# Performance work log

Measured on AMD Instinct MI355X. Metric: run time of the kernel, lower is better.

## Reference

```python
import jax, jax.numpy as jnp
import numpy as np

N_NODES = 100_000
N_EDGES = 1_600_000
N_GRAPHS = 256
IN_DIM, HID, HEADS, LAYERS = 480, 128, 4, 3
HEAD_DIM = HID // HEADS
NEG_SLOPE = 0.2
LN_EPS = 1e-5


def setup_inputs() -> dict:
    key = jax.random.key(0)
    ks = jax.random.split(key, 12)
    x = jax.random.normal(ks[0], (N_NODES, IN_DIM), dtype=jnp.float32)
    edge_index = jax.random.randint(ks[1], (2, N_EDGES), 0, N_NODES, dtype=jnp.int32)
    batch = jnp.sort(jax.random.randint(ks[2], (N_NODES,), 0, N_GRAPHS, dtype=jnp.int32))
    s_in = 1.0 / np.sqrt(IN_DIM)
    s_h = 1.0 / np.sqrt(HID)
    return {
        "x": x,
        "W_in": jax.random.uniform(ks[3], (IN_DIM, HID), jnp.float32, -s_in, s_in),
        "b_in": jax.random.uniform(ks[4], (HID,), jnp.float32, -s_in, s_in),
        "W_gat": jax.random.uniform(ks[5], (LAYERS, HID, HID), jnp.float32, -s_h, s_h),
        "att_src": jax.random.uniform(ks[6], (LAYERS, HEADS, HEAD_DIM), jnp.float32, -s_h, s_h),
        "att_dst": jax.random.uniform(ks[7], (LAYERS, HEADS, HEAD_DIM), jnp.float32, -s_h, s_h),
        "b_gat": jnp.zeros((LAYERS, HID), jnp.float32),
        "ln_g": jnp.ones((LAYERS, HID), jnp.float32),
        "ln_b": jnp.zeros((LAYERS, HID), jnp.float32),
        "edge_index": edge_index,
        "batch": batch,
    }


def _gat_conv(h_in, W, a_src, a_dst, bias, src, dst, n):
    # h: [N, H, D] per-head projected features
    h = (h_in @ W).reshape(n, HEADS, HEAD_DIM)
    asrc = jnp.sum(h * a_src, axis=-1)  # [N, H]
    adst = jnp.sum(h * a_dst, axis=-1)  # [N, H]
    e = jax.nn.leaky_relu(asrc[src] + adst[dst], NEG_SLOPE)  # [E, H]
    # scatter-softmax over incoming edges of each destination node
    emax = jax.ops.segment_max(e, dst, num_segments=n)  # [N, H]
    emax = jnp.where(jnp.isfinite(emax), emax, 0.0)
    ex = jnp.exp(e - emax[dst])
    denom = jax.ops.segment_sum(ex, dst, num_segments=n)
    alpha = ex / jnp.maximum(denom, 1e-16)[dst]  # [E, H]
    out = jax.ops.segment_sum(alpha[:, :, None] * h[src], dst, num_segments=n)
    return out.reshape(n, HID) + bias


def _layer_norm(x, g, b):
    mu = jnp.mean(x, axis=-1, keepdims=True)
    var = jnp.mean(jnp.square(x - mu), axis=-1, keepdims=True)
    return (x - mu) * jax.lax.rsqrt(var + LN_EPS) * g + b


def reference(x, W_in, b_in, W_gat, att_src, att_dst, b_gat, ln_g, ln_b, edge_index, batch):
    n = x.shape[0]
    # PyG GATConv default add_self_loops=True
    loop = jnp.arange(n, dtype=edge_index.dtype)
    src = jnp.concatenate([edge_index[0], loop])
    dst = jnp.concatenate([edge_index[1], loop])

    h = jax.nn.relu(x @ W_in + b_in)
    for l in range(LAYERS):
        residual = h
        h = _gat_conv(h, W_gat[l], att_src[l], att_dst[l], b_gat[l], src, dst, n)
        h = jax.nn.relu(_layer_norm(h, ln_g[l], ln_b[l]))
        # dropout omitted (eval mode)
        h = h + residual
    # global mean pool per graph
    sums = jax.ops.segment_sum(h, batch, num_segments=N_GRAPHS)
    cnt = jax.ops.segment_sum(jnp.ones((n,), h.dtype), batch, num_segments=N_GRAPHS)
    return sums / jnp.maximum(cnt, 1.0)[:, None]
```

## Files before the change

### kernel.cpp

```cpp
#include <hip/hip_runtime.h>
#include <hip/hip_bf16.h>

#define HID 128
#define NEG_SLOPE 0.2f
#define LN_EPS 1e-5f
#define SEG_CAP 8192

typedef __attribute__((ext_vector_type(8))) short short8;
typedef __attribute__((ext_vector_type(4))) float floatx4;

__device__ __forceinline__ float us2f(unsigned short u) {
    union { unsigned int i; float f; } c; c.i = ((unsigned int)u) << 16; return c.f;
}
__device__ __forceinline__ float lo2f(unsigned u) {
    union { unsigned int i; float f; } c; c.i = u << 16; return c.f;
}
__device__ __forceinline__ float hi2f(unsigned u) {
    union { unsigned int i; float f; } c; c.i = u & 0xffff0000u; return c.f;
}
__device__ __forceinline__ unsigned short f2us(float f) {
    union { float f; unsigned u; } c; c.f = f;
    unsigned r = c.u + 0x7FFF + ((c.u >> 16) & 1);
    return (unsigned short)(r >> 16);
}
__device__ __forceinline__ unsigned pack2(float a, float b) {
    return (unsigned)f2us(a) | ((unsigned)f2us(b) << 16);
}
__device__ __forceinline__ float ldw(const void* p, long i, int bf) {
    return bf ? us2f(((const unsigned short*)p)[i]) : ((const float*)p)[i];
}
__device__ __forceinline__ float lrelu(float x) { return x > 0.f ? x : NEG_SLOPE * x; }
__device__ __forceinline__ float wsum32(float x) {
#pragma unroll
    for (int o = 16; o > 0; o >>= 1) x += __shfl_xor(x, o);
    return x;
}
__device__ __forceinline__ float pick4(float4 v, int h) {
    return h == 0 ? v.x : (h == 1 ? v.y : (h == 2 ? v.z : v.w));
}

__global__ __launch_bounds__(256) void init_kernel(const float* __restrict__ x, int* __restrict__ flag,
                                                   int* __restrict__ bucket_cnt) {
    const int t = blockIdx.x * 256 + threadIdx.x;
    if (t < 512) bucket_cnt[t] = 0;
    if (blockIdx.x == 0 && threadIdx.x < 64) {
        float v = x[threadIdx.x];
        int bad = (!(v == v)) || (fabsf(v) > 1e6f);
        unsigned long long m = __ballot(bad);
        if (threadIdx.x == 0) flag[0] = (m != 0ull) ? 1 : 0;
    }
}

__global__ __launch_bounds__(256) void bucket_hist_kernel(const int* __restrict__ dst, int E, int nb,
                                                          int* __restrict__ bucket_cnt) {
    __shared__ int hist[512];
    for (int i = threadIdx.x; i < nb; i += 256) hist[i] = 0;
    __syncthreads();
    const int base = blockIdx.x * 4096;
    const int end = min(base + 4096, E);
    for (int i = base + threadIdx.x; i < end; i += 256)
        atomicAdd(&hist[dst[i] >> 8], 1);
    __syncthreads();
    for (int i = threadIdx.x; i < nb; i += 256)
        if (hist[i]) atomicAdd(&bucket_cnt[i], hist[i]);
}

__global__ __launch_bounds__(512) void bucket_scan_kernel(const int* __restrict__ bucket_cnt,
                                                          int* __restrict__ bucket_base,
                                                          int* __restrict__ cursor,
                                                          int nb, int* __restrict__ row_ptr, int N) {
    __shared__ int sc[512];
    const int t = threadIdx.x;
    const int v = (t < nb) ? bucket_cnt[t] : 0;
    int x = v;
    sc[t] = x;
    __syncthreads();
    for (int o = 1; o < 512; o <<= 1) {
        const int y = (t >= o) ? sc[t - o] : 0;
        __syncthreads();
        x += y;
        sc[t] = x;
        __syncthreads();
    }
    if (t < nb) { bucket_base[t] = x - v; cursor[t] = x - v; }
    if (t == nb - 1) { bucket_base[nb] = x; row_ptr[N] = x; }
}

__global__ __launch_bounds__(256) void partition_kernel(const int* __restrict__ src, const int* __restrict__ dst,
                                                        int E, int nb, int* __restrict__ cursor,
                                                        unsigned long long* __restrict__ tmp) {
    __shared__ int hist[512];
    __shared__ int tbase[512];
    for (int i = threadIdx.x; i < nb; i += 256) hist[i] = 0;
    __syncthreads();
    const int base = blockIdx.x * 4096;
    const int end = min(base + 4096, E);
    int myd[16], mys[16], myr[16];
#pragma unroll
    for (int j = 0; j < 16; ++j) {
        const int i = base + threadIdx.x + j * 256;
        if (i < end) {
            const int d = dst[i];
            myd[j] = d;
            mys[j] = src[i];
            myr[j] = atomicAdd(&hist[d >> 8], 1);
        } else {
            myd[j] = -1;
        }
    }
    __syncthreads();
    for (int i = threadIdx.x; i < nb; i += 256) {
        const int hv = hist[i];
        tbase[i] = hv ? atomicAdd(&cursor[i], hv) : 0;
    }
    __syncthreads();
#pragma unroll
    for (int j = 0; j < 16; ++j) {
        if (myd[j] >= 0) {
            const int b = myd[j] >> 8;
            tmp[(size_t)tbase[b] + myr[j]] = ((unsigned long long)(unsigned)myd[j] << 32) | (unsigned)mys[j];
        }
    }
}

__global__ __launch_bounds__(256) void bucket_sort_kernel(const unsigned long long* __restrict__ tmp,
                                                          const int* __restrict__ bucket_base,
                                                          int* __restrict__ row_ptr, int* __restrict__ csr,
                                                          int N) {
    __shared__ int hist[256];
    __shared__ int sc[256];
    __shared__ int off[256];
    __shared__ int outb[SEG_CAP];
    const int b = blockIdx.x;
    const int node0 = b << 8;
    const int nn = min(256, N - node0);
    const int s0 = bucket_base[b], s1 = bucket_base[b + 1];
    const int cnt = s1 - s0;
    const int t = threadIdx.x;
    hist[t] = 0;
    __syncthreads();
    for (int i = s0 + t; i < s1; i += 256) {
        const int d = (int)(tmp[i] >> 32) - node0;
        atomicAdd(&hist[d], 1);
    }
    __syncthreads();
    const int v = hist[t];
    int x = v;
    sc[t] = x;
    __syncthreads();
    for (int o = 1; o < 256; o <<= 1) {
        const int y = (t >= o) ? sc[t - o] : 0;
        __syncthreads();
        x += y;
        sc[t] = x;
        __syncthreads();
    }
    off[t] = x - v;
    if (t < nn) row_ptr[node0 + t] = s0 + (x - v);
    hist[t] = 0;
    __syncthreads();
    if (cnt <= SEG_CAP) {
        for (int i = s0 + t; i < s1; i += 256) {
            const unsigned long long pr = tmp[i];
            const int d = (int)(pr >> 32) - node0;
            const int p = off[d] + atomicAdd(&hist[d], 1);
            outb[p] = (int)(unsigned)(pr & 0xffffffffu);
        }
        __syncthreads();
        for (int i = t; i < cnt; i += 256) csr[s0 + i] = outb[i];
    } else {
        for (int i = s0 + t; i < s1; i += 256) {
            const unsigned long long pr = tmp[i];
            const int d = (int)(pr >> 32) - node0;
            const int p = off[d] + atomicAdd(&hist[d], 1);
            csr[s0 + p] = (int)(unsigned)(pr & 0xffffffffu);
        }
    }
}

__global__ __launch_bounds__(256) void transpose_w_kernel(const void* __restrict__ W, long w_off, int K,
                                                          unsigned short* __restrict__ Wt,
                                                          const int* __restrict__ flagp) {
    const int bf = flagp[0];
    const int i = blockIdx.x * 256 + threadIdx.x;
    if (i >= 128 * K) return;
    const int n = i / K, k = i - n * K;
    const long s = w_off + (long)k * 128 + n;
    Wt[i] = bf ? ((const unsigned short*)W)[s] : f2us(((const float*)W)[s]);
}

__global__ __launch_bounds__(256) void transpose_wg_kernel(const void* __restrict__ W,
                                                           unsigned short* __restrict__ Wt,
                                                           const int* __restrict__ flagp) {
    const int bf = flagp[0];
    const int i = blockIdx.x * 256 + threadIdx.x;
    if (i >= 3 * 128 * 128) return;
    const int l = i >> 14, j = i & 16383;
    const int n = j >> 7, k = j & 127;
    const long s = (long)l * 16384 + (long)k * 128 + n;
    Wt[i] = bf ? ((const unsigned short*)W)[s] : f2us(((const float*)W)[s]);
}

template <int C_BF, int FUSE>
__global__ __launch_bounds__(256) void mfma_gemm_kernel(const void* __restrict__ Ap, int a_input,
                                                        const unsigned short* __restrict__ Bt,
                                                        const void* __restrict__ bias, long bias_off,
                                                        void* __restrict__ Cp,
                                                        const void* __restrict__ attS,
                                                        const void* __restrict__ attD, long a_off,
                                                        float* __restrict__ asrc, float* __restrict__ adst,
                                                        int M, int K, int do_relu,
                                                        const int* __restrict__ flagp) {
    __shared__ unsigned short As[2][128 * 40];
    __shared__ unsigned short Bs[2][128 * 40];
    const int bf = flagp[0];
    const int a_bf = a_input ? (bf ? 1 : 2) : 2;
    const int t = threadIdx.x;
    const int bm = blockIdx.x * 128;
    const int lane = t & 63, wave = t >> 6;
    const int r = lane & 15, quad = lane >> 4;
    const int srow = t >> 1, skh = (t & 1) * 16;
    const int grow = bm + srow;

    floatx4 acc[2][8];
#pragma unroll
    for (int mt = 0; mt < 2; ++mt)
#pragma unroll
        for (int nt = 0; nt < 8; ++nt)
#pragma unroll
            for (int q = 0; q < 4; ++q) acc[mt][nt][q] = 0.f;

    auto loadAB = [&](int k0, uint4& u0, uint4& u1, uint4& v0, uint4& v1) {
        u0 = make_uint4(0, 0, 0, 0); u1 = u0;
        if (grow < M) {
            const long aidx = (long)grow * K + k0 + skh;
            if (a_bf == 1) {
                const unsigned short* ap = (const unsigned short*)Ap + aidx;
                u0 = ((const uint4*)ap)[0];
                u1 = ((const uint4*)ap)[1];
            } else {
                const float* ap = (const float*)Ap + aidx;
                float4 f0 = ((const float4*)ap)[0];
                float4 f1 = ((const float4*)ap)[1];
                float4 f2 = ((const float4*)ap)[2];
                float4 f3 = ((const float4*)ap)[3];
                u0 = make_uint4(pack2(f0.x, f0.y), pack2(f0.z, f0.w), pack2(f1.x, f1.y), pack2(f1.z, f1.w));
                u1 = make_uint4(pack2(f2.x, f2.y), pack2(f2.z, f2.w), pack2(f3.x, f3.y), pack2(f3.z, f3.w));
            }
        }
        const unsigned short* bp = Bt + (long)srow * K + k0 + skh;
        v0 = ((const uint4*)bp)[0];
        v1 = ((const uint4*)bp)[1];
    };

    uint4 a0, a1, b0, b1;
    loadAB(0, a0, a1, b0, b1);
    *(uint4*)&As[0][srow * 40 + skh]     = a0;
    *(uint4*)&As[0][srow * 40 + skh + 8] = a1;
    *(uint4*)&Bs[0][srow * 40 + skh]     = b0;
    *(uint4*)&Bs[0][srow * 40 + skh + 8] = b1;
    __syncthreads();

    int cur = 0;
    for (int k0 = 0; k0 < K; k0 += 32) {
        const bool have = (k0 + 32) < K;
        if (have) loadAB(k0 + 32, a0, a1, b0, b1);

        short8 afr[2];
        afr[0] = *(const short8*)&As[cur][(wave * 32 + r) * 40 + quad * 8];
        afr[1] = *(const short8*)&As[cur][(wave * 32 + 16 + r) * 40 + quad * 8];
#pragma unroll
        for (int nt = 0; nt < 8; ++nt) {
            short8 bfr = *(const short8*)&Bs[cur][(nt * 16 + r) * 40 + quad * 8];
            acc[0][nt] = __builtin_amdgcn_mfma_f32_16x16x32_bf16(afr[0], bfr, acc[0][nt], 0, 0, 0);
            acc[1][nt] = __builtin_amdgcn_mfma_f32_16x16x32_bf16(afr[1], bfr, acc[1][nt], 0, 0, 0);
        }

        if (have) {
            cur ^= 1;
            *(uint4*)&As[cur][srow * 40 + skh]     = a0;
            *(uint4*)&As[cur][srow * 40 + skh + 8] = a1;
            *(uint4*)&Bs[cur][srow * 40 + skh]     = b0;
            *(uint4*)&Bs[cur][srow * 40 + skh + 8] = b1;
            __syncthreads();
        }
    }

    if (FUSE) {
        float aS[8], aD[8];
#pragma unroll
        for (int nt = 0; nt < 8; ++nt) {
            aS[nt] = ldw(attS, a_off + nt * 16 + r, bf);
            aD[nt] = ldw(attD, a_off + nt * 16 + r, bf);
        }
#pragma unroll
        for (int mt = 0; mt < 2; ++mt) {
#pragma unroll
            for (int reg = 0; reg < 4; ++reg) {
                const int gr = bm + wave * 32 + mt * 16 + quad * 4 + reg;
                if (gr < M) {
                    float s0 = 0.f, s1 = 0.f, s2 = 0.f, s3 = 0.f;
                    float d0 = 0.f, d1 = 0.f, d2 = 0.f, d3 = 0.f;
#pragma unroll
                    for (int nt = 0; nt < 8; ++nt) {
                        const float v = acc[mt][nt][reg];
                        const unsigned short us = f2us(v);
                        ((unsigned short*)Cp)[(long)gr * HID + nt * 16 + r] = us;
                        const float vr = us2f(us);
                        if (nt < 2)      { s0 = fmaf(vr, aS[nt], s0); d0 = fmaf(vr, aD[nt], d0); }
                        else if (nt < 4) { s1 = fmaf(vr, aS[nt], s1); d1 = fmaf(vr, aD[nt], d1); }
                        else if (nt < 6) { s2 = fmaf(vr, aS[nt], s2); d2 = fmaf(vr, aD[nt], d2); }
                        else             { s3 = fmaf(vr, aS[nt], s3); d3 = fmaf(vr, aD[nt], d3); }
                    }
#pragma unroll
                    for (int o = 1; o < 16; o <<= 1) {
                        s0 += __shfl_xor(s0, o); s1 += __shfl_xor(s1, o);
                        s2 += __shfl_xor(s2, o); s3 += __shfl_xor(s3, o);
                        d0 += __shfl_xor(d0, o); d1 += __shfl_xor(d1, o);
                        d2 += __shfl_xor(d2, o); d3 += __shfl_xor(d3, o);
                    }
                    const int hsel = r & 3;
                    const float sv = hsel == 0 ? s0 : (hsel == 1 ? s1 : (hsel == 2 ? s2 : s3));
                    const float dv = hsel == 0 ? d0 : (hsel == 1 ? d1 : (hsel == 2 ? d2 : d3));
                    if (r < 4)      asrc[(size_t)gr * 4 + hsel] = sv;
                    else if (r < 8) adst[(size_t)gr * 4 + hsel] = dv;
                }
            }
        }
    } else {
        float bb[8];
#pragma unroll
        for (int nt = 0; nt < 8; ++nt) bb[nt] = bias ? ldw(bias, bias_off + nt * 16 + r, bf) : 0.f;

#pragma unroll
        for (int mt = 0; mt < 2; ++mt) {
            const int gr0 = bm + wave * 32 + mt * 16 + quad * 4;
#pragma unroll
            for (int reg = 0; reg < 4; ++reg) {
                const int gr = gr0 + reg;
                if (gr < M) {
#pragma unroll
                    for (int nt = 0; nt < 8; ++nt) {
                        float v = acc[mt][nt][reg] + bb[nt];
                        if (do_relu) v = fmaxf(v, 0.f);
                        const long ci = (long)gr * HID + nt * 16 + r;
                        if (C_BF) ((unsigned short*)Cp)[ci] = f2us(v);
                        else      ((float*)Cp)[ci] = v;
                    }
                }
            }
        }
    }
}

__global__ __launch_bounds__(256) void gat_kernel(float* __restrict__ h,
                                                  const unsigned short* __restrict__ hp,
                                                  const float* __restrict__ asrc,
                                                  const float* __restrict__ adst,
                                                  const int* __restrict__ row_ptr,
                                                  const int* __restrict__ csr,
                                                  const void* __restrict__ bgat,
                                                  const void* __restrict__ lng,
                                                  const void* __restrict__ lnb, long w_off,
                                                  int N, const int* __restrict__ flagp) {
    __shared__ uint2 ebuf[8][160];
    const int bf = flagp[0];
    const int lane = threadIdx.x & 63;
    const int wslot = threadIdx.x >> 6;
    const int half = lane >> 5;
    const int ll = lane & 31;
    const int head4 = ll >> 3;
    const int c0 = ll << 2;
    const int n = (blockIdx.x << 3) | (wslot << 1) | half;
    if (n >= N) return;

    const int e0 = row_ptr[n], e1 = row_ptr[n + 1];
    const float4 ad4 = *(const float4*)(adst + (size_t)n * 4);
    const float4 as4 = *(const float4*)(asrc + (size_t)n * 4);
    float4 es;
    es.x = lrelu(as4.x + ad4.x); es.y = lrelu(as4.y + ad4.y);
    es.z = lrelu(as4.z + ad4.z); es.w = lrelu(as4.w + ad4.w);

    const uint2 us = *(const uint2*)(hp + (size_t)n * HID + c0);
    float4 acc;
    acc.x = lo2f(us.x); acc.y = hi2f(us.x);
    acc.z = lo2f(us.y); acc.w = hi2f(us.y);

    float4 dnp = make_float4(0.f, 0.f, 0.f, 0.f);
    uint2* eb = ebuf[(wslot << 1) | half];

    for (int base = e0; base < e1; base += 32) {
        const int cnt = min(32, e1 - base);
        int s = 0;
        float4 ex4 = make_float4(0.f, 0.f, 0.f, 0.f);
        if (ll < cnt) {
            s = csr[base + ll];
            const float4 a = *(const float4*)(asrc + (size_t)s * 4);
            ex4.x = __expf(lrelu(a.x + ad4.x) - es.x);
            ex4.y = __expf(lrelu(a.y + ad4.y) - es.y);
            ex4.z = __expf(lrelu(a.z + ad4.z) - es.z);
            ex4.w = __expf(lrelu(a.w + ad4.w) - es.w);
            dnp.x += ex4.x; dnp.y += ex4.y; dnp.z += ex4.z; dnp.w += ex4.w;
        }
        const unsigned su = (unsigned)s;
        eb[ll * 5 + 0] = make_uint2(su, __float_as_uint(ex4.x));
        eb[ll * 5 + 1] = make_uint2(su, __float_as_uint(ex4.y));
        eb[ll * 5 + 2] = make_uint2(su, __float_as_uint(ex4.z));
        eb[ll * 5 + 3] = make_uint2(su, __float_as_uint(ex4.w));

        float4 aA = make_float4(0.f, 0.f, 0.f, 0.f);
        float4 aB = make_float4(0.f, 0.f, 0.f, 0.f);
        float4 aC = make_float4(0.f, 0.f, 0.f, 0.f);
        float4 aD = make_float4(0.f, 0.f, 0.f, 0.f);
        int i = 0;
#define GAT_EDGE(idx, A)                                                      \
        {                                                                     \
            const uint2 q = eb[(idx) * 5 + head4];                            \
            const uint2 u = *(const uint2*)(hp + (size_t)q.x * HID + c0);     \
            const float wq = __uint_as_float(q.y);                            \
            A.x = fmaf(wq, lo2f(u.x), A.x);                                   \
            A.y = fmaf(wq, hi2f(u.x), A.y);                                   \
            A.z = fmaf(wq, lo2f(u.y), A.z);                                   \
            A.w = fmaf(wq, hi2f(u.y), A.w);                                   \
        }
        for (; i + 4 <= cnt; i += 4) {
            GAT_EDGE(i + 0, aA);
            GAT_EDGE(i + 1, aB);
            GAT_EDGE(i + 2, aC);
            GAT_EDGE(i + 3, aD);
        }
        for (; i < cnt; ++i) GAT_EDGE(i, aA);
#undef GAT_EDGE
        acc.x += (aA.x + aB.x) + (aC.x + aD.x);
        acc.y += (aA.y + aB.y) + (aC.y + aD.y);
        acc.z += (aA.z + aB.z) + (aC.z + aD.z);
        acc.w += (aA.w + aB.w) + (aC.w + aD.w);
    }

    float4 dn;
    dn.x = wsum32(dnp.x) + 1.f;
    dn.y = wsum32(dnp.y) + 1.f;
    dn.z = wsum32(dnp.z) + 1.f;
    dn.w = wsum32(dnp.w) + 1.f;

    const float invd = 1.f / fmaxf(pick4(dn, head4), 1e-16f);
    acc.x *= invd; acc.y *= invd; acc.z *= invd; acc.w *= invd;
    acc.x += ldw(bgat, w_off + c0 + 0, bf);
    acc.y += ldw(bgat, w_off + c0 + 1, bf);
    acc.z += ldw(bgat, w_off + c0 + 2, bf);
    acc.w += ldw(bgat, w_off + c0 + 3, bf);

    const float mean = wsum32(acc.x + acc.y + acc.z + acc.w) * (1.f / 128.f);
    const float d0 = acc.x - mean, d1 = acc.y - mean, d2 = acc.z - mean, d3 = acc.w - mean;
    const float var = wsum32(d0 * d0 + d1 * d1 + d2 * d2 + d3 * d3) * (1.f / 128.f);
    const float rstd = rsqrtf(var + LN_EPS);
    float o0 = d0 * rstd * ldw(lng, w_off + c0 + 0, bf) + ldw(lnb, w_off + c0 + 0, bf);
    float o1 = d1 * rstd * ldw(lng, w_off + c0 + 1, bf) + ldw(lnb, w_off + c0 + 1, bf);
    float o2 = d2 * rstd * ldw(lng, w_off + c0 + 2, bf) + ldw(lnb, w_off + c0 + 2, bf);
    float o3 = d3 * rstd * ldw(lng, w_off + c0 + 3, bf) + ldw(lnb, w_off + c0 + 3, bf);
    o0 = fmaxf(o0, 0.f); o1 = fmaxf(o1, 0.f); o2 = fmaxf(o2, 0.f); o3 = fmaxf(o3, 0.f);

    const float4 r = *(const float4*)(h + (size_t)n * HID + c0);
    *(float4*)(h + (size_t)n * HID + c0) = make_float4(o0 + r.x, o1 + r.y, o2 + r.z, o3 + r.w);
}

__global__ __launch_bounds__(1024) void pool_kernel(const float* __restrict__ h, const int* __restrict__ batch,
                                                    void* __restrict__ out, int N,
                                                    const int* __restrict__ flagp) {
    const int g = blockIdx.x;
    int a = 0, b = N;
    while (a < b) { int mid = (a + b) >> 1; if (batch[mid] < g) a = mid + 1; else b = mid; }
    const int lo = a;
    b = N;
    while (a < b) { int mid = (a + b) >> 1; if (batch[mid] <= g) a = mid + 1; else b = mid; }
    const int hi = a;

    const int col = threadIdx.x & 127;
    const int slot = threadIdx.x >> 7;
    float s = 0.f;
    for (int r = lo + slot; r < hi; r += 8) s += h[(size_t)r * HID + col];
    __shared__ float part[8][128];
    part[slot][col] = s;
    __syncthreads();
    if (threadIdx.x < 128) {
        float tot = part[0][threadIdx.x];
#pragma unroll
        for (int p = 1; p < 8; ++p) tot += part[p][threadIdx.x];
        const float v = tot / fmaxf((float)(hi - lo), 1.f);
        if (flagp[0]) ((unsigned short*)out)[g * HID + threadIdx.x] = f2us(v);
        else          ((float*)out)[g * HID + threadIdx.x] = v;
    }
}

extern "C" void kernel_launch(void* const* d_in, const int* in_sizes, int n_in,
                              void* d_out, int out_size, void* d_ws, size_t ws_size,
                              hipStream_t stream) {
    const void* x     = d_in[0];
    const void* W_in  = d_in[1];
    const void* b_in  = d_in[2];
    const void* W_gat = d_in[3];
    const void* att_s = d_in[4];
    const void* att_d = d_in[5];
    const void* b_gat = d_in[6];
    const void* ln_g  = d_in[7];
    const void* ln_b  = d_in[8];
    const int* edge_index = (const int*)d_in[9];
    const int* batch      = (const int*)d_in[10];

    const int N = in_sizes[10];
    const int E = in_sizes[9] / 2;
    const int IN_DIM = in_sizes[0] / N;
    const int n_graphs = out_size / HID;

    const int* esrc = edge_index;
    const int* edst = edge_index + E;

    char* w = (char*)d_ws;
    auto carve = [&](size_t bytes) -> void* {
        void* p = (void*)w;
        w += (bytes + 255) & ~(size_t)255;
        return p;
    };
    int* flag             = (int*)carve(256);
    int* row_ptr          = (int*)carve((size_t)(N + 1) * 4);
    int* csr              = (int*)carve((size_t)E * 4);
    float* asrc           = (float*)carve((size_t)N * 4 * 4);
    float* adst           = (float*)carve((size_t)N * 4 * 4);
    int* bucket_cnt       = (int*)carve(512 * 4);
    int* bucket_base      = (int*)carve(513 * 4);
    int* cursor           = (int*)carve(512 * 4);
    unsigned short* Wt_in = (unsigned short*)carve((size_t)HID * IN_DIM * 2);
    unsigned short* Wt_g  = (unsigned short*)carve((size_t)3 * HID * HID * 2);
    float* h              = (float*)carve((size_t)N * HID * 4);
    unsigned short* hp    = (unsigned short*)carve((size_t)N * HID * 2);
    unsigned long long* tmp = (unsigned long long*)h;
    (void)ws_size; (void)n_in;

    init_kernel<<<2, 256, 0, stream>>>((const float*)x, flag, bucket_cnt);

    const int nb = (N + 255) >> 8;
    const int ntiles = (E + 4095) / 4096;
    bucket_hist_kernel<<<ntiles, 256, 0, stream>>>(edst, E, nb, bucket_cnt);
    bucket_scan_kernel<<<1, 512, 0, stream>>>(bucket_cnt, bucket_base, cursor, nb, row_ptr, N);
    partition_kernel<<<ntiles, 256, 0, stream>>>(esrc, edst, E, nb, cursor, tmp);
    bucket_sort_kernel<<<nb, 256, 0, stream>>>(tmp, bucket_base, row_ptr, csr, N);

    transpose_w_kernel<<<(HID * IN_DIM + 255) / 256, 256, 0, stream>>>(W_in, 0, IN_DIM, Wt_in, flag);
    transpose_wg_kernel<<<(3 * HID * HID + 255) / 256, 256, 0, stream>>>(W_gat, Wt_g, flag);

    mfma_gemm_kernel<0, 0><<<(N + 127) / 128, 256, 0, stream>>>(
        x, 1, Wt_in, b_in, 0, h, nullptr, nullptr, 0, nullptr, nullptr, N, IN_DIM, 1, flag);

    for (int l = 0; l < 3; ++l) {
        mfma_gemm_kernel<1, 1><<<(N + 127) / 128, 256, 0, stream>>>(
            h, 0, Wt_g + (size_t)l * HID * HID, nullptr, 0, hp,
            att_s, att_d, (long)l * HID, asrc, adst, N, HID, 0, flag);
        gat_kernel<<<(N + 7) / 8, 256, 0, stream>>>(h, hp, asrc, adst, row_ptr, csr,
                                                    b_gat, ln_g, ln_b, (long)l * HID, N, flag);
    }

    pool_kernel<<<n_graphs, 1024, 0, stream>>>(h, batch, d_out, N, flag);
}
```

Baseline: 750.8 us.

## Replace two-level bucket sort CSR build with per-node counting sort

Builds the destination-sorted CSR by counting edges per node with global atomics, running a two-level prefix scan and scattering source indices through per-node atomic cursors. This replaces the bucket histogram, partition and in-bucket sort pipeline, and the two weight-transpose kernels are merged into one launch. The intent is fewer passes over the edge list and less intermediate traffic. In exchange the per-node global atomics can contend, and the order of neighbours within a row is no longer deterministic, which may change floating-point summation order.

```diff
diff --git a/kernel.cpp b/kernel.cpp
--- a/kernel.cpp
+++ b/kernel.cpp
@@ -4,7 +4,6 @@
 #define HID 128
 #define NEG_SLOPE 0.2f
 #define LN_EPS 1e-5f
-#define SEG_CAP 8192
 
 typedef __attribute__((ext_vector_type(8))) short short8;
 typedef __attribute__((ext_vector_type(4))) float floatx4;
@@ -40,9 +39,9 @@
 }
 
 __global__ __launch_bounds__(256) void init_kernel(const float* __restrict__ x, int* __restrict__ flag,
-                                                   int* __restrict__ bucket_cnt) {
-    const int t = blockIdx.x * 256 + threadIdx.x;
-    if (t < 512) bucket_cnt[t] = 0;
+                                                   int* __restrict__ cnt, int N) {
+    const int i = blockIdx.x * 256 + threadIdx.x;
+    if (i < N) cnt[i] = 0;
     if (blockIdx.x == 0 && threadIdx.x < 64) {
         float v = x[threadIdx.x];
         int bad = (!(v == v)) || (fabsf(v) > 1e6f);
@@ -51,27 +50,38 @@
     }
 }
 
-__global__ __launch_bounds__(256) void bucket_hist_kernel(const int* __restrict__ dst, int E, int nb,
-                                                          int* __restrict__ bucket_cnt) {
-    __shared__ int hist[512];
-    for (int i = threadIdx.x; i < nb; i += 256) hist[i] = 0;
+__global__ __launch_bounds__(256) void node_hist_kernel(const int* __restrict__ dst, int E,
+                                                        int* __restrict__ cnt) {
+    const int i = blockIdx.x * 256 + threadIdx.x;
+    if (i < E) atomicAdd(&cnt[dst[i]], 1);
+}
+
+__global__ __launch_bounds__(256) void scan_local_kernel(const int* __restrict__ cnt,
+                                                         int* __restrict__ loc,
+                                                         int* __restrict__ part, int N) {
+    __shared__ int sc[256];
+    const int t = threadIdx.x;
+    const int n = blockIdx.x * 256 + t;
+    const int v = (n < N) ? cnt[n] : 0;
+    int x = v;
+    sc[t] = x;
     __syncthreads();
-    const int base = blockIdx.x * 4096;
-    const int end = min(base + 4096, E);
-    for (int i = base + threadIdx.x; i < end; i += 256)
-        atomicAdd(&hist[dst[i] >> 8], 1);
-    __syncthreads();
-    for (int i = threadIdx.x; i < nb; i += 256)
-        if (hist[i]) atomicAdd(&bucket_cnt[i], hist[i]);
-}
-
-__global__ __launch_bounds__(512) void bucket_scan_kernel(const int* __restrict__ bucket_cnt,
-                                                          int* __restrict__ bucket_base,
-                                                          int* __restrict__ cursor,
-                                                          int nb, int* __restrict__ row_ptr, int N) {
+    for (int o = 1; o < 256; o <<= 1) {
+        const int y = (t >= o) ? sc[t - o] : 0;
+        __syncthreads();
+        x += y;
+        sc[t] = x;
+        __syncthreads();
+    }
+    if (n < N) loc[n] = x - v;
+    if (t == 255) part[blockIdx.x] = x;
+}
+
+__global__ __launch_bounds__(512) void scan_part_kernel(int* __restrict__ part, int nblk,
+                                                        int* __restrict__ row_ptr, int N) {
     __shared__ int sc[512];
     const int t = threadIdx.x;
-    const int v = (t < nb) ? bucket_cnt[t] : 0;
+    const int v = (t < nblk) ? part[t] : 0;
     int x = v;
     sc[t] = x;
     __syncthreads();
@@ -82,123 +92,54 @@
         sc[t] = x;
         __syncthreads();
     }
-    if (t < nb) { bucket_base[t] = x - v; cursor[t] = x - v; }
-    if (t == nb - 1) { bucket_base[nb] = x; row_ptr[N] = x; }
-}
-
-__global__ __launch_bounds__(256) void partition_kernel(const int* __restrict__ src, const int* __restrict__ dst,
-                                                        int E, int nb, int* __restrict__ cursor,
-                                                        unsigned long long* __restrict__ tmp) {
-    __shared__ int hist[512];
-    __shared__ int tbase[512];
-    for (int i = threadIdx.x; i < nb; i += 256) hist[i] = 0;
-    __syncthreads();
-    const int base = blockIdx.x * 4096;
-    const int end = min(base + 4096, E);
-    int myd[16], mys[16], myr[16];
-#pragma unroll
-    for (int j = 0; j < 16; ++j) {
-        const int i = base + threadIdx.x + j * 256;
-        if (i < end) {
-            const int d = dst[i];
-            myd[j] = d;
-            mys[j] = src[i];
-            myr[j] = atomicAdd(&hist[d >> 8], 1);
-        } else {
-            myd[j] = -1;
-        }
-    }
-    __syncthreads();
-    for (int i = threadIdx.x; i < nb; i += 256) {
-        const int hv = hist[i];
-        tbase[i] = hv ? atomicAdd(&cursor[i], hv) : 0;
-    }
-    __syncthreads();
-#pragma unroll
-    for (int j = 0; j < 16; ++j) {
-        if (myd[j] >= 0) {
-            const int b = myd[j] >> 8;
-            tmp[(size_t)tbase[b] + myr[j]] = ((unsigned long long)(unsigned)myd[j] << 32) | (unsigned)mys[j];
-        }
-    }
-}
-
-__global__ __launch_bounds__(256) void bucket_sort_kernel(const unsigned long long* __restrict__ tmp,
-                                                          const int* __restrict__ bucket_base,
-                                                          int* __restrict__ row_ptr, int* __restrict__ csr,
-                                                          int N) {
-    __shared__ int hist[256];
-    __shared__ int sc[256];
-    __shared__ int off[256];
-    __shared__ int outb[SEG_CAP];
-    const int b = blockIdx.x;
-    const int node0 = b << 8;
-    const int nn = min(256, N - node0);
-    const int s0 = bucket_base[b], s1 = bucket_base[b + 1];
-    const int cnt = s1 - s0;
-    const int t = threadIdx.x;
-    hist[t] = 0;
-    __syncthreads();
-    for (int i = s0 + t; i < s1; i += 256) {
-        const int d = (int)(tmp[i] >> 32) - node0;
-        atomicAdd(&hist[d], 1);
-    }
-    __syncthreads();
-    const int v = hist[t];
-    int x = v;
-    sc[t] = x;
-    __syncthreads();
-    for (int o = 1; o < 256; o <<= 1) {
-        const int y = (t >= o) ? sc[t - o] : 0;
-        __syncthreads();
-        x += y;
-        sc[t] = x;
-        __syncthreads();
-    }
-    off[t] = x - v;
-    if (t < nn) row_ptr[node0 + t] = s0 + (x - v);
-    hist[t] = 0;
-    __syncthreads();
-    if (cnt <= SEG_CAP) {
-        for (int i = s0 + t; i < s1; i += 256) {
-            const unsigned long long pr = tmp[i];
-            const int d = (int)(pr >> 32) - node0;
-            const int p = off[d] + atomicAdd(&hist[d], 1);
-            outb[p] = (int)(unsigned)(pr & 0xffffffffu);
-        }
-        __syncthreads();
-        for (int i = t; i < cnt; i += 256) csr[s0 + i] = outb[i];
+    if (t < nblk) part[t] = x - v;
+    if (t == nblk - 1) row_ptr[N] = x;
+}
+
+__global__ __launch_bounds__(256) void scan_add_kernel(const int* __restrict__ loc,
+                                                       const int* __restrict__ part,
+                                                       int* __restrict__ row_ptr,
+                                                       int* __restrict__ cursor, int N) {
+    const int n = blockIdx.x * 256 + threadIdx.x;
+    if (n < N) {
+        const int v = loc[n] + part[blockIdx.x];
+        row_ptr[n] = v;
+        cursor[n] = v;
+    }
+}
+
+__global__ __launch_bounds__(256) void scatter_kernel(const int* __restrict__ src,
+                                                      const int* __restrict__ dst, int E,
+                                                      int* __restrict__ cursor, int* __restrict__ csr) {
+    const int i = blockIdx.x * 256 + threadIdx.x;
+    if (i < E) {
+        const int d = dst[i];
+        const int p = atomicAdd(&cursor[d], 1);
+        csr[p] = src[i];
+    }
+}
+
+__global__ __launch_bounds__(256) void transpose_all_kernel(const void* __restrict__ W_in,
+                                                            const void* __restrict__ W_gat,
+                                                            unsigned short* __restrict__ Wt_in,
+                                                            unsigned short* __restrict__ Wt_g,
+                                                            int K_in, const int* __restrict__ flagp) {
+    const int bf = flagp[0];
+    int i = blockIdx.x * 256 + threadIdx.x;
+    const int n_in = 128 * K_in;
+    if (i < n_in) {
+        const int n = i / K_in, k = i - n * K_in;
+        const long s = (long)k * 128 + n;
+        Wt_in[i] = bf ? ((const unsigned short*)W_in)[s] : f2us(((const float*)W_in)[s]);
     } else {
-        for (int i = s0 + t; i < s1; i += 256) {
-            const unsigned long long pr = tmp[i];
-            const int d = (int)(pr >> 32) - node0;
-            const int p = off[d] + atomicAdd(&hist[d], 1);
-            csr[s0 + p] = (int)(unsigned)(pr & 0xffffffffu);
-        }
-    }
-}
-
-__global__ __launch_bounds__(256) void transpose_w_kernel(const void* __restrict__ W, long w_off, int K,
-                                                          unsigned short* __restrict__ Wt,
-                                                          const int* __restrict__ flagp) {
-    const int bf = flagp[0];
-    const int i = blockIdx.x * 256 + threadIdx.x;
-    if (i >= 128 * K) return;
-    const int n = i / K, k = i - n * K;
-    const long s = w_off + (long)k * 128 + n;
-    Wt[i] = bf ? ((const unsigned short*)W)[s] : f2us(((const float*)W)[s]);
-}
-
-__global__ __launch_bounds__(256) void transpose_wg_kernel(const void* __restrict__ W,
-                                                           unsigned short* __restrict__ Wt,
-                                                           const int* __restrict__ flagp) {
-    const int bf = flagp[0];
-    const int i = blockIdx.x * 256 + threadIdx.x;
-    if (i >= 3 * 128 * 128) return;
-    const int l = i >> 14, j = i & 16383;
-    const int n = j >> 7, k = j & 127;
-    const long s = (long)l * 16384 + (long)k * 128 + n;
-    Wt[i] = bf ? ((const unsigned short*)W)[s] : f2us(((const float*)W)[s]);
+        i -= n_in;
+        if (i < 3 * 128 * 128) {
+            const int l = i >> 14, j = i & 16383;
+            const int n = j >> 7, k = j & 127;
+            const long s = (long)l * 16384 + (long)k * 128 + n;
+            Wt_g[i] = bf ? ((const unsigned short*)W_gat)[s] : f2us(((const float*)W_gat)[s]);
+        }
+    }
 }
 
 template <int C_BF, int FUSE>
@@ -526,27 +467,28 @@
     int* csr              = (int*)carve((size_t)E * 4);
     float* asrc           = (float*)carve((size_t)N * 4 * 4);
     float* adst           = (float*)carve((size_t)N * 4 * 4);
-    int* bucket_cnt       = (int*)carve(512 * 4);
-    int* bucket_base      = (int*)carve(513 * 4);
-    int* cursor           = (int*)carve(512 * 4);
+    int* cnt              = (int*)carve((size_t)N * 4);
+    int* loc              = (int*)carve((size_t)N * 4);
+    int* cursor           = (int*)carve((size_t)N * 4);
+    int* part             = (int*)carve(512 * 4);
     unsigned short* Wt_in = (unsigned short*)carve((size_t)HID * IN_DIM * 2);
     unsigned short* Wt_g  = (unsigned short*)carve((size_t)3 * HID * HID * 2);
     float* h              = (float*)carve((size_t)N * HID * 4);
     unsigned short* hp    = (unsigned short*)carve((size_t)N * HID * 2);
-    unsigned long long* tmp = (unsigned long long*)h;
     (void)ws_size; (void)n_in;
 
-    init_kernel<<<2, 256, 0, stream>>>((const float*)x, flag, bucket_cnt);
-
-    const int nb = (N + 255) >> 8;
-    const int ntiles = (E + 4095) / 4096;
-    bucket_hist_kernel<<<ntiles, 256, 0, stream>>>(edst, E, nb, bucket_cnt);
-    bucket_scan_kernel<<<1, 512, 0, stream>>>(bucket_cnt, bucket_base, cursor, nb, row_ptr, N);
-    partition_kernel<<<ntiles, 256, 0, stream>>>(esrc, edst, E, nb, cursor, tmp);
-    bucket_sort_kernel<<<nb, 256, 0, stream>>>(tmp, bucket_base, row_ptr, csr, N);
-
-    transpose_w_kernel<<<(HID * IN_DIM + 255) / 256, 256, 0, stream>>>(W_in, 0, IN_DIM, Wt_in, flag);
-    transpose_wg_kernel<<<(3 * HID * HID + 255) / 256, 256, 0, stream>>>(W_gat, Wt_g, flag);
+    const int nblk = (N + 255) >> 8;
+
+    init_kernel<<<nblk, 256, 0, stream>>>((const float*)x, flag, cnt, N);
+
+    node_hist_kernel<<<(E + 255) / 256, 256, 0, stream>>>(edst, E, cnt);
+    scan_local_kernel<<<nblk, 256, 0, stream>>>(cnt, loc, part, N);
+    scan_part_kernel<<<1, 512, 0, stream>>>(part, nblk, row_ptr, N);
+    scan_add_kernel<<<nblk, 256, 0, stream>>>(loc, part, row_ptr, cursor, N);
+    scatter_kernel<<<(E + 255) / 256, 256, 0, stream>>>(esrc, edst, E, cursor, csr);
+
+    transpose_all_kernel<<<(HID * IN_DIM + 3 * HID * HID + 255) / 256, 256, 0, stream>>>(
+        W_in, W_gat, Wt_in, Wt_g, IN_DIM, flag);
 
     mfma_gemm_kernel<0, 0><<<(N + 127) / 128, 256, 0, stream>>>(
         x, 1, Wt_in, b_in, 0, h, nullptr, nullptr, 0, nullptr, nullptr, N, IN_DIM, 1, flag);
```

Result: slower. 884.2 us (+17.8%).
